# Optimization experiments

Hardware: AMD Instinct MI355X
Metric: run time of the kernel (lower is better)

The kernel has to match this reference:

```python
import jax, jax.numpy as jnp
import numpy as np


def _build_schedule(N, M):
    """Round-robin (circle-method) tournament schedule of Givens rotations.

    Returns per-round, per-row arrays (R=N-1 rounds, each with N/2 disjoint pairs):
      partner[r, n]: row paired with n in round r (self if inactive)
      tpos[r, n]   : flat theta index for the pair (i<j: i*(N-1)-i*(i-1)/2 + j-i-1)
      sign[r, n]   : -1 for the lower-index row i, +1 for j, 0 if inactive
      active[r, n] : 1.0 if row participates in a rotation this round
    Pairs with min(i,j) >= M carry no theta and are skipped (identity).
    """
    assert N % 2 == 0, "even N assumed for the tournament schedule"
    R = N - 1
    players = list(range(N))
    partner = np.tile(np.arange(N, dtype=np.int32), (R, 1))
    tpos = np.zeros((R, N), np.int32)
    sign = np.zeros((R, N), np.float32)
    active = np.zeros((R, N), np.float32)
    for r in range(R):
        for k in range(N // 2):
            a, b = players[k], players[N - 1 - k]
            i, j = (a, b) if a < b else (b, a)
            if i >= M:
                continue
            t = i * (N - 1) - i * (i - 1) // 2 + (j - i - 1)
            partner[r, i], partner[r, j] = j, i
            tpos[r, i] = tpos[r, j] = t
            sign[r, i], sign[r, j] = -1.0, 1.0
            active[r, i] = active[r, j] = 1.0
        players = [players[0], players[-1]] + players[1:-1]
    return (jnp.asarray(partner), jnp.asarray(tpos),
            jnp.asarray(sign), jnp.asarray(active))


def _rotmat_forward(x, thetas, M=None):
    # x: [N, B]; applies the product of Givens rotations G(i,j,theta) round by round.
    N = x.shape[0]
    M = N if M is None else M
    sched = _build_schedule(N, M)

    def body(xc, rd):
        p, t, sg, ac = rd
        th = thetas[t]                       # [N]
        c = jnp.where(ac > 0, jnp.cos(th), 1.0)
        s = sg * jnp.sin(th)                 # 0 where inactive
        # row i: c*x[i] - s*x[j]; row j: s*x[i] + c*x[j]
        return c[:, None] * xc + s[:, None] * xc[p], None

    out, _ = jax.lax.scan(body, x, sched)
    return out


def setup_inputs() -> dict:
    key = jax.random.key(0)
    k1, k2 = jax.random.split(key)
    N, B = 512, 1024
    n_theta = N * (N - 1) // 2  # 130816 (M == N)
    x = jax.random.normal(k1, (N, B), dtype=jnp.float32)
    thetas = jax.random.normal(k2, (n_theta,), dtype=jnp.float32)
    return {"x": x, "thetas": thetas}


def reference(x, thetas):
    return _rotmat_forward(x, thetas)
```

## Files before the change

kernel.cpp:

```cpp
#include <hip/hip_runtime.h>
#include <hip/hip_fp16.h>


#define N_COLS   1024
#define PAIRS    256

typedef __attribute__((ext_vector_type(4))) float f32x4;

__global__ __launch_bounds__(256) void rotmat_setup(const float* __restrict__ thetas,
                                                    __half2* __restrict__ cs16) {
    const int r = blockIdx.x;
    const int k = threadIdx.x;
    int pu = (k == 0) ? 0 : ((k - 1 - r + 1022) % 511) + 1;
    int pv = ((510 - k - r + 1022) % 511) + 1;
    int i = min(pu, pv), j = max(pu, pv);
    int t = i * 511 - (i * (i - 1)) / 2 + (j - i - 1);
    float s, c;
    sincosf(thetas[t], &s, &c);
    float sp = (pu < pv) ? s : -s;
    cs16[r * 256 + k] = __floats2half2_rn(c, sp);
}

__device__ __forceinline__ float dpp_shr1(float old, float src) {
    return __int_as_float(__builtin_amdgcn_update_dpp(
        __float_as_int(old), __float_as_int(src), 0x138, 0xF, 0xF, false));
}
__device__ __forceinline__ float dpp_shl1(float old, float src) {
    return __int_as_float(__builtin_amdgcn_update_dpp(
        __float_as_int(old), __float_as_int(src), 0x130, 0xF, 0xF, false));
}

__device__ __forceinline__ void glds16(const void* g, void* l) {
    __builtin_amdgcn_global_load_lds(
        (const __attribute__((address_space(1))) void*)g,
        (__attribute__((address_space(3))) void*)l, 16, 0, 0);
}

#define FMIX_SN(d, P, x)                                                      \
    asm("v_fma_mix_f32 %0, -%1, %2, 0 op_sel:[1,0,0] op_sel_hi:[1,0,0]"       \
        : "=v"(d) : "v"(P), "v"(x));
#define FMIX_SP(d, P, x)                                                      \
    asm("v_fma_mix_f32 %0, %1, %2, 0 op_sel:[1,0,0] op_sel_hi:[1,0,0]"        \
        : "=v"(d) : "v"(P), "v"(x));
#define FMIX_C(d, P, x, a)                                                    \
    asm("v_fma_mix_f32 %0, %1, %2, %3 op_sel:[0,0,0] op_sel_hi:[1,0,0]"       \
        : "=v"(d) : "v"(P), "v"(x), "v"(a));

#define ROUND(AA)                                                  \
    {                                                              \
        float P0 = (AA).x, P1 = (AA).y, P2 = (AA).z, P3 = (AA).w;  \
        float t3, u3, l3, h3, t0, u0, l0, h0;                      \
        FMIX_SN(t3, P3, hi[3])                                     \
        FMIX_C(l3, P3, lo[3], t3)                                  \
        FMIX_SP(u3, P3, lo[3])                                     \
        FMIX_C(h3, P3, hi[3], u3)                                  \
        FMIX_SN(t0, P0, hi[0])                                     \
        FMIX_C(l0, P0, lo[0], t0)                                  \
        FMIX_SP(u0, P0, lo[0])                                     \
        FMIX_C(h0, P0, hi[0], u0)                                  \
        float nlo0 = dpp_shr1(l0, l3);                             \
        float nhi3 = dpp_shl1(l3, h0);                             \
        float t1, u1, l1, h1, t2, u2, l2, h2;                      \
        FMIX_SN(t1, P1, hi[1])                                     \
        FMIX_C(l1, P1, lo[1], t1)                                  \
        FMIX_SP(u1, P1, lo[1])                                     \
        FMIX_C(h1, P1, hi[1], u1)                                  \
        FMIX_SN(t2, P2, hi[2])                                     \
        FMIX_C(l2, P2, lo[2], t2)                                  \
        FMIX_SP(u2, P2, lo[2])                                     \
        FMIX_C(h2, P2, hi[2], u2)                                  \
        float nlo1 = is0 ? h0 : l0;                                \
        lo[0] = nlo0; lo[1] = nlo1; lo[2] = l1; lo[3] = l2;        \
        hi[0] = h1; hi[1] = h2; hi[2] = h3; hi[3] = nhi3;          \
    }

#define DSRD(dst, addr, imm)                                   \
    asm volatile("ds_read_b128 %0, %1 offset:%c2"              \
                 : "=v"(dst) : "v"(addr), "i"(imm))

#define WL3(a) asm volatile("s_waitcnt lgkmcnt(3)" : "+v"(a))
#define WL2(a) asm volatile("s_waitcnt lgkmcnt(2)" : "+v"(a))
#define WL1(a) asm volatile("s_waitcnt lgkmcnt(1)" : "+v"(a))
#define WL0(a) asm volatile("s_waitcnt lgkmcnt(0)" : "+v"(a))

#define WAITV(n) asm volatile("s_waitcnt vmcnt(" #n ")" ::: "memory")
#define BAR()                               \
    __builtin_amdgcn_s_barrier();           \
    __builtin_amdgcn_sched_barrier(0)

#define STAGE(cix, bix)                                              \
    {                                                                \
        const char* g_ = gsrc + (size_t)(cix)*16384;                 \
        char* l_ = lb + (size_t)(bix)*16384;                         \
        _Pragma("unroll")                                            \
        for (int j = 0; j < 4; ++j)                                  \
            glds16(g_ + j * 1024, l_ + j * 1024);                    \
    }

#define CHUNK16(ACUR, ANXT)                                    \
    WL3(A0); ROUND(A0) DSRD(A0, ACUR,  4 * 1024);              \
    WL3(A1); ROUND(A1) DSRD(A1, ACUR,  5 * 1024);              \
    WL3(A2); ROUND(A2) DSRD(A2, ACUR,  6 * 1024);              \
    WL3(A3); ROUND(A3) DSRD(A3, ACUR,  7 * 1024);              \
    WL3(A0); ROUND(A0) DSRD(A0, ACUR,  8 * 1024);              \
    WL3(A1); ROUND(A1) DSRD(A1, ACUR,  9 * 1024);              \
    WL3(A2); ROUND(A2) DSRD(A2, ACUR, 10 * 1024);              \
    WL3(A3); ROUND(A3) DSRD(A3, ACUR, 11 * 1024);              \
    WL3(A0); ROUND(A0) DSRD(A0, ACUR, 12 * 1024);              \
    WL3(A1); ROUND(A1) DSRD(A1, ACUR, 13 * 1024);              \
    WL3(A2); ROUND(A2) DSRD(A2, ACUR, 14 * 1024);              \
    WL3(A3); ROUND(A3) DSRD(A3, ACUR, 15 * 1024);              \
    WL3(A0); ROUND(A0) DSRD(A0, ANXT,  0 * 1024);              \
    WL3(A1); ROUND(A1) DSRD(A1, ANXT,  1 * 1024);              \
    WL3(A2); ROUND(A2) DSRD(A2, ANXT,  2 * 1024);              \
    WL3(A3); ROUND(A3) DSRD(A3, ANXT,  3 * 1024);

template <bool TAB>
__global__ __launch_bounds__(256, 1) void rotmat_main(const float* __restrict__ x,
                                                      const float* __restrict__ thetas,
                                                      const __half2* __restrict__ cs16,
                                                      float* __restrict__ out) {
    __shared__ f32x4 tab[3 * 1024];

    const int lane = threadIdx.x & 63;
    const int wave = threadIdx.x >> 6;
    const int col  = (blockIdx.x << 2) + wave;
    const int k0   = lane << 2;
    const bool is0 = (lane == 0);

    float lo[4], hi[4];
#pragma unroll
    for (int m = 0; m < 4; ++m) {
        lo[m] = x[(k0 + m) * N_COLS + col];
        hi[m] = x[(511 - k0 - m) * N_COLS + col];
    }

    if constexpr (TAB) {
        const char* gsrc = (const char*)cs16 + (size_t)wave * 4096 + (size_t)lane * 16;
        char* lb = (char*)(&tab[0]) + (size_t)wave * 4096;
        unsigned ldsLane;
        {
            auto p3 = (__attribute__((address_space(3))) char*)(&tab[0]);
            ldsLane = (unsigned)(size_t)p3 + (unsigned)(lane * 16);
        }

        f32x4 A0, A1, A2, A3;

        STAGE(0, 0)
        STAGE(1, 1)
        WAITV(0);
        BAR();
        {
            unsigned a0 = ldsLane;
            DSRD(A0, a0, 0 * 1024);
            DSRD(A1, a0, 1 * 1024);
            DSRD(A2, a0, 2 * 1024);
            DSRD(A3, a0, 3 * 1024);
        }

        int bufCur = 0, bufNxt = 1, bufStg = 2;
        for (int c = 0; c < 30; ++c) {
            WAITV(0);
            BAR();
            STAGE(c + 2, bufStg)
            unsigned aCur = ldsLane + (unsigned)bufCur * 16384u;
            unsigned aNxt = ldsLane + (unsigned)bufNxt * 16384u;
            CHUNK16(aCur, aNxt)
            int t_ = bufCur; bufCur = bufNxt; bufNxt = bufStg; bufStg = t_;
        }

        {
            WAITV(0);
            BAR();
            unsigned aCur = ldsLane + (unsigned)bufCur * 16384u;
            unsigned aNxt = ldsLane + (unsigned)bufNxt * 16384u;
            CHUNK16(aCur, aNxt)
            int t_ = bufCur; bufCur = bufNxt; bufNxt = bufStg; bufStg = t_;
        }

        {
            unsigned aCur = ldsLane + (unsigned)bufCur * 16384u;
            WL3(A0); ROUND(A0) DSRD(A0, aCur,  4 * 1024);
            WL3(A1); ROUND(A1) DSRD(A1, aCur,  5 * 1024);
            WL3(A2); ROUND(A2) DSRD(A2, aCur,  6 * 1024);
            WL3(A3); ROUND(A3) DSRD(A3, aCur,  7 * 1024);
            WL3(A0); ROUND(A0) DSRD(A0, aCur,  8 * 1024);
            WL3(A1); ROUND(A1) DSRD(A1, aCur,  9 * 1024);
            WL3(A2); ROUND(A2) DSRD(A2, aCur, 10 * 1024);
            WL3(A3); ROUND(A3) DSRD(A3, aCur, 11 * 1024);
            WL3(A0); ROUND(A0) DSRD(A0, aCur, 12 * 1024);
            WL3(A1); ROUND(A1) DSRD(A1, aCur, 13 * 1024);
            WL3(A2); ROUND(A2) DSRD(A2, aCur, 14 * 1024);
            WL3(A3); ROUND(A3)
            WL2(A0); ROUND(A0)
            WL1(A1); ROUND(A1)
            WL0(A2); ROUND(A2)
        }
    } else {
        int pu[4], pv[4];
#pragma unroll
        for (int m = 0; m < 4; ++m) {
            pu[m] = (k0 + m == 0) ? 0 : (k0 + m);
            pv[m] = 511 - (k0 + m);
        }
        for (int r = 0; r < 511; ++r) {
            float cc[4], ss[4];
#pragma unroll
            for (int m = 0; m < 4; ++m) {
                int i = min(pu[m], pv[m]), j = max(pu[m], pv[m]);
                int t = i * 511 - (i * (i - 1)) / 2 + (j - i - 1);
                float s, c;
                sincosf(thetas[t], &s, &c);
                cc[m] = c;
                ss[m] = (pu[m] < pv[m]) ? s : -s;
            }
            {
                float t3 = ss[3] * hi[3], u3 = ss[3] * lo[3];
                float l3 = fmaf(cc[3], lo[3], -t3);
                float h3 = fmaf(cc[3], hi[3], u3);
                float t0 = ss[0] * hi[0], u0 = ss[0] * lo[0];
                float l0 = fmaf(cc[0], lo[0], -t0);
                float h0 = fmaf(cc[0], hi[0], u0);
                float nlo0 = dpp_shr1(l0, l3);
                float nhi3 = dpp_shl1(l3, h0);
                float t1 = ss[1] * hi[1], u1 = ss[1] * lo[1];
                float l1 = fmaf(cc[1], lo[1], -t1);
                float h1 = fmaf(cc[1], hi[1], u1);
                float t2 = ss[2] * hi[2], u2 = ss[2] * lo[2];
                float l2 = fmaf(cc[2], lo[2], -t2);
                float h2 = fmaf(cc[2], hi[2], u2);
                float nlo1 = is0 ? h0 : l0;
                lo[0] = nlo0; lo[1] = nlo1; lo[2] = l1; lo[3] = l2;
                hi[0] = h1; hi[1] = h2; hi[2] = h3; hi[3] = nhi3;
            }
#pragma unroll
            for (int m = 0; m < 4; ++m) {
                pu[m] = (k0 + m == 0) ? 0 : ((pu[m] == 1) ? 511 : pu[m] - 1);
                pv[m] = (pv[m] == 1) ? 511 : pv[m] - 1;
            }
        }
    }

#pragma unroll
    for (int m = 0; m < 4; ++m) {
        out[(k0 + m) * N_COLS + col]       = lo[m];
        out[(511 - k0 - m) * N_COLS + col] = hi[m];
    }
}

extern "C" void kernel_launch(void* const* d_in, const int* in_sizes, int n_in,
                              void* d_out, int out_size, void* d_ws, size_t ws_size,
                              hipStream_t stream) {
    const float* x  = (const float*)d_in[0];
    const float* th = (const float*)d_in[1];
    float* out      = (float*)d_out;

    const size_t need = (size_t)512 * 1024;
    if (ws_size >= need) {
        __half2* cs16 = (__half2*)d_ws;
        rotmat_setup<<<511, PAIRS, 0, stream>>>(th, cs16);
        rotmat_main<true><<<N_COLS / 4, 256, 0, stream>>>(x, th, cs16, out);
    } else {
        rotmat_main<false><<<N_COLS / 4, 256, 0, stream>>>(x, th, nullptr, out);
    }
}
```

Baseline: 46.42 us.

## Decompose rotation sequence into two dense orthogonal matrices applied by GEMM

Instead of streaming all 511 rounds of Givens rotations over each of the 1024 columns, the new path builds two 512x512 orthogonal matrices, one per half of the rounds, by running the rotation rounds on identity columns in parallel (1024 waves). It then applies them to x with two fp32 tiled GEMMs, and a final kernel applies the last round directly. The goal is to expose more parallelism than the column-serial main kernel and turn the work into GEMM-shaped compute. The cost is extra kernel launches, an extra intermediate buffer, fp32 GEMM work of about 0.5 GFLOP per pass without matrix cores, and a different rounding order.

```diff
diff --git a/kernel.cpp b/kernel.cpp
--- a/kernel.cpp
+++ b/kernel.cpp
@@ -29,7 +29,6 @@
     return __int_as_float(__builtin_amdgcn_update_dpp(
         __float_as_int(old), __float_as_int(src), 0x130, 0xF, 0xF, false));
 }
-
 __device__ __forceinline__ void glds16(const void* g, void* l) {
     __builtin_amdgcn_global_load_lds(
         (const __attribute__((address_space(1))) void*)g,
@@ -77,12 +76,10 @@
 #define DSRD(dst, addr, imm)                                   \
     asm volatile("ds_read_b128 %0, %1 offset:%c2"              \
                  : "=v"(dst) : "v"(addr), "i"(imm))
-
 #define WL3(a) asm volatile("s_waitcnt lgkmcnt(3)" : "+v"(a))
 #define WL2(a) asm volatile("s_waitcnt lgkmcnt(2)" : "+v"(a))
 #define WL1(a) asm volatile("s_waitcnt lgkmcnt(1)" : "+v"(a))
 #define WL0(a) asm volatile("s_waitcnt lgkmcnt(0)" : "+v"(a))
-
 #define WAITV(n) asm volatile("s_waitcnt vmcnt(" #n ")" ::: "memory")
 #define BAR()                               \
     __builtin_amdgcn_s_barrier();           \
@@ -93,8 +90,8 @@
         const char* g_ = gsrc + (size_t)(cix)*16384;                 \
         char* l_ = lb + (size_t)(bix)*16384;                         \
         _Pragma("unroll")                                            \
-        for (int j = 0; j < 4; ++j)                                  \
-            glds16(g_ + j * 1024, l_ + j * 1024);                    \
+        for (int j_ = 0; j_ < 4; ++j_)                               \
+            glds16(g_ + j_ * 1024, l_ + j_ * 1024);                  \
     }
 
 #define CHUNK16(ACUR, ANXT)                                    \
@@ -115,6 +112,171 @@
     WL3(A2); ROUND(A2) DSRD(A2, ANXT,  2 * 1024);              \
     WL3(A3); ROUND(A3) DSRD(A3, ANXT,  3 * 1024);
 
+#define CHUNK15_TAIL(ACUR)                                     \
+    WL3(A0); ROUND(A0) DSRD(A0, ACUR,  4 * 1024);              \
+    WL3(A1); ROUND(A1) DSRD(A1, ACUR,  5 * 1024);              \
+    WL3(A2); ROUND(A2) DSRD(A2, ACUR,  6 * 1024);              \
+    WL3(A3); ROUND(A3) DSRD(A3, ACUR,  7 * 1024);              \
+    WL3(A0); ROUND(A0) DSRD(A0, ACUR,  8 * 1024);              \
+    WL3(A1); ROUND(A1) DSRD(A1, ACUR,  9 * 1024);              \
+    WL3(A2); ROUND(A2) DSRD(A2, ACUR, 10 * 1024);              \
+    WL3(A3); ROUND(A3) DSRD(A3, ACUR, 11 * 1024);              \
+    WL3(A0); ROUND(A0) DSRD(A0, ACUR, 12 * 1024);              \
+    WL3(A1); ROUND(A1) DSRD(A1, ACUR, 13 * 1024);              \
+    WL3(A2); ROUND(A2) DSRD(A2, ACUR, 14 * 1024);              \
+    WL3(A3); ROUND(A3)                                         \
+    WL2(A0); ROUND(A0)                                         \
+    WL1(A1); ROUND(A1)                                         \
+    WL0(A2); ROUND(A2)
+
+__device__ __forceinline__ int player_of(int r, int p) {
+    return (p == 0) ? 0 : ((p - 1 - r + 1022) % 511) + 1;
+}
+
+__global__ __launch_bounds__(256, 1) void rotmat_build(const __half2* __restrict__ cs16,
+                                                       float* __restrict__ qt) {
+    __shared__ f32x4 tab[3 * 1024];
+
+    const int lane = threadIdx.x & 63;
+    const int wave = threadIdx.x >> 6;
+    const int wid  = (blockIdx.x << 2) + wave;
+    const int seg  = wid >> 9;
+    const int j    = wid & 511;
+    const int r0   = seg ? 255 : 0;
+    const int k0   = lane << 2;
+    const bool is0 = (lane == 0);
+
+    float lo[4], hi[4];
+#pragma unroll
+    for (int m = 0; m < 4; ++m) {
+        int p = k0 + m, pq = 511 - p;
+        lo[m] = (player_of(r0, p) == j) ? 1.0f : 0.0f;
+        hi[m] = (player_of(r0, pq) == j) ? 1.0f : 0.0f;
+    }
+
+    const char* gsrc = (const char*)cs16 + (size_t)r0 * 1024
+                     + (size_t)wave * 4096 + (size_t)lane * 16;
+    char* lb = (char*)(&tab[0]) + (size_t)wave * 4096;
+    unsigned ldsLane;
+    {
+        auto p3 = (__attribute__((address_space(3))) char*)(&tab[0]);
+        ldsLane = (unsigned)(size_t)p3 + (unsigned)(lane * 16);
+    }
+
+    f32x4 A0, A1, A2, A3;
+
+    STAGE(0, 0)
+    STAGE(1, 1)
+    WAITV(0);
+    BAR();
+    {
+        unsigned a0 = ldsLane;
+        DSRD(A0, a0, 0 * 1024);
+        DSRD(A1, a0, 1 * 1024);
+        DSRD(A2, a0, 2 * 1024);
+        DSRD(A3, a0, 3 * 1024);
+    }
+
+    int bufCur = 0, bufNxt = 1, bufStg = 2;
+    for (int c = 0; c < 14; ++c) {
+        WAITV(0);
+        BAR();
+        STAGE(c + 2, bufStg)
+        unsigned aCur = ldsLane + (unsigned)bufCur * 16384u;
+        unsigned aNxt = ldsLane + (unsigned)bufNxt * 16384u;
+        CHUNK16(aCur, aNxt)
+        int t_ = bufCur; bufCur = bufNxt; bufNxt = bufStg; bufStg = t_;
+    }
+    {
+        WAITV(0);
+        BAR();
+        unsigned aCur = ldsLane + (unsigned)bufCur * 16384u;
+        unsigned aNxt = ldsLane + (unsigned)bufNxt * 16384u;
+        CHUNK16(aCur, aNxt)
+        int t_ = bufCur; bufCur = bufNxt; bufNxt = bufStg; bufStg = t_;
+    }
+    {
+        unsigned aCur = ldsLane + (unsigned)bufCur * 16384u;
+        CHUNK15_TAIL(aCur)
+    }
+
+    const int r1 = seg ? 510 : 255;
+    float* qv = qt + (size_t)seg * 262144 + (size_t)j * 512;
+#pragma unroll
+    for (int m = 0; m < 4; ++m) {
+        int p = k0 + m, pq = 511 - p;
+        qv[player_of(r1, p)]  = lo[m];
+        qv[player_of(r1, pq)] = hi[m];
+    }
+}
+
+__global__ __launch_bounds__(256) void gemm_qt(const float* __restrict__ AT,
+                                               const float* __restrict__ B,
+                                               float* __restrict__ C) {
+    __shared__ float As[32][32];
+    __shared__ float Bs[32][64];
+
+    const int t    = threadIdx.x;
+    const int bx   = blockIdx.x & 15;
+    const int by   = blockIdx.x >> 4;
+    const int row0 = by * 32, col0 = bx * 64;
+    const int mr   = (t & 15) * 2;
+    const int nc   = (t >> 4) * 4;
+
+    float acc00 = 0, acc01 = 0, acc02 = 0, acc03 = 0;
+    float acc10 = 0, acc11 = 0, acc12 = 0, acc13 = 0;
+
+    for (int kt = 0; kt < 16; ++kt) {
+        __syncthreads();
+        {
+            int kk = t >> 3, mm = (t & 7) * 4;
+            *(float4*)&As[kk][mm] =
+                *(const float4*)&AT[(size_t)(kt * 32 + kk) * 512 + row0 + mm];
+        }
+        {
+            int kk = t >> 4, cc = (t & 15) * 4;
+            *(float4*)&Bs[kk][cc] =
+                *(const float4*)&B[(size_t)(kt * 32 + kk) * 1024 + col0 + cc];
+            *(float4*)&Bs[kk + 16][cc] =
+                *(const float4*)&B[(size_t)(kt * 32 + kk + 16) * 1024 + col0 + cc];
+        }
+        __syncthreads();
+#pragma unroll
+        for (int kk = 0; kk < 32; ++kk) {
+            float a0 = As[kk][mr], a1 = As[kk][mr + 1];
+            float4 b = *(float4*)&Bs[kk][nc];
+            acc00 = fmaf(a0, b.x, acc00); acc01 = fmaf(a0, b.y, acc01);
+            acc02 = fmaf(a0, b.z, acc02); acc03 = fmaf(a0, b.w, acc03);
+            acc10 = fmaf(a1, b.x, acc10); acc11 = fmaf(a1, b.y, acc11);
+            acc12 = fmaf(a1, b.z, acc12); acc13 = fmaf(a1, b.w, acc13);
+        }
+    }
+    *(float4*)&C[(size_t)(row0 + mr) * 1024 + col0 + nc] =
+        make_float4(acc00, acc01, acc02, acc03);
+    *(float4*)&C[(size_t)(row0 + mr + 1) * 1024 + col0 + nc] =
+        make_float4(acc10, acc11, acc12, acc13);
+}
+
+__global__ __launch_bounds__(256) void round_last(const float* __restrict__ thetas,
+                                                  float* __restrict__ out) {
+    const int k = blockIdx.x;
+    int pu = (k == 0) ? 0 : ((k - 1 - 510 + 1022) % 511) + 1;
+    int pv = ((510 - k - 510 + 1022) % 511) + 1;
+    int i = min(pu, pv), jj = max(pu, pv);
+    int t = i * 511 - (i * (i - 1)) / 2 + (jj - i - 1);
+    float s, c;
+    sincosf(thetas[t], &s, &c);
+    float* ri = out + (size_t)i * 1024;
+    float* rj = out + (size_t)jj * 1024;
+#pragma unroll
+    for (int u = 0; u < 4; ++u) {
+        int col = threadIdx.x + u * 256;
+        float a = ri[col], b = rj[col];
+        ri[col] = fmaf(c, a, -(s * b));
+        rj[col] = fmaf(s, a, c * b);
+    }
+}
+
 template <bool TAB>
 __global__ __launch_bounds__(256, 1) void rotmat_main(const float* __restrict__ x,
                                                       const float* __restrict__ thetas,
@@ -143,9 +305,7 @@
             auto p3 = (__attribute__((address_space(3))) char*)(&tab[0]);
             ldsLane = (unsigned)(size_t)p3 + (unsigned)(lane * 16);
         }
-
         f32x4 A0, A1, A2, A3;
-
         STAGE(0, 0)
         STAGE(1, 1)
         WAITV(0);
@@ -157,7 +317,6 @@
             DSRD(A2, a0, 2 * 1024);
             DSRD(A3, a0, 3 * 1024);
         }
-
         int bufCur = 0, bufNxt = 1, bufStg = 2;
         for (int c = 0; c < 30; ++c) {
             WAITV(0);
@@ -168,7 +327,6 @@
             CHUNK16(aCur, aNxt)
             int t_ = bufCur; bufCur = bufNxt; bufNxt = bufStg; bufStg = t_;
         }
-
         {
             WAITV(0);
             BAR();
@@ -177,24 +335,9 @@
             CHUNK16(aCur, aNxt)
             int t_ = bufCur; bufCur = bufNxt; bufNxt = bufStg; bufStg = t_;
         }
-
         {
             unsigned aCur = ldsLane + (unsigned)bufCur * 16384u;
-            WL3(A0); ROUND(A0) DSRD(A0, aCur,  4 * 1024);
-            WL3(A1); ROUND(A1) DSRD(A1, aCur,  5 * 1024);
-            WL3(A2); ROUND(A2) DSRD(A2, aCur,  6 * 1024);
-            WL3(A3); ROUND(A3) DSRD(A3, aCur,  7 * 1024);
-            WL3(A0); ROUND(A0) DSRD(A0, aCur,  8 * 1024);
-            WL3(A1); ROUND(A1) DSRD(A1, aCur,  9 * 1024);
-            WL3(A2); ROUND(A2) DSRD(A2, aCur, 10 * 1024);
-            WL3(A3); ROUND(A3) DSRD(A3, aCur, 11 * 1024);
-            WL3(A0); ROUND(A0) DSRD(A0, aCur, 12 * 1024);
-            WL3(A1); ROUND(A1) DSRD(A1, aCur, 13 * 1024);
-            WL3(A2); ROUND(A2) DSRD(A2, aCur, 14 * 1024);
-            WL3(A3); ROUND(A3)
-            WL2(A0); ROUND(A0)
-            WL1(A1); ROUND(A1)
-            WL0(A2); ROUND(A2)
+            CHUNK15_TAIL(aCur)
         }
     } else {
         int pu[4], pv[4];
@@ -207,8 +350,8 @@
             float cc[4], ss[4];
 #pragma unroll
             for (int m = 0; m < 4; ++m) {
-                int i = min(pu[m], pv[m]), j = max(pu[m], pv[m]);
-                int t = i * 511 - (i * (i - 1)) / 2 + (j - i - 1);
+                int i = min(pu[m], pv[m]), jj = max(pu[m], pv[m]);
+                int t = i * 511 - (i * (i - 1)) / 2 + (jj - i - 1);
                 float s, c;
                 sincosf(thetas[t], &s, &c);
                 cc[m] = c;
@@ -255,8 +398,21 @@
     const float* th = (const float*)d_in[1];
     float* out      = (float*)d_out;
 
-    const size_t need = (size_t)512 * 1024;
-    if (ws_size >= need) {
+    const size_t TAB_B = (size_t)512 * 1024;
+    const size_t Q_B   = (size_t)512 * 512 * 4;
+    const size_t Y_B   = (size_t)512 * 1024 * 4;
+    const size_t need_decomp = TAB_B + 2 * Q_B + Y_B;
+
+    if (ws_size >= need_decomp) {
+        __half2* cs16 = (__half2*)d_ws;
+        float* qt = (float*)((char*)d_ws + TAB_B);
+        float* Y  = (float*)((char*)d_ws + TAB_B + 2 * Q_B);
+        rotmat_setup<<<511, PAIRS, 0, stream>>>(th, cs16);
+        rotmat_build<<<256, 256, 0, stream>>>(cs16, qt);
+        gemm_qt<<<256, 256, 0, stream>>>(qt, x, Y);
+        gemm_qt<<<256, 256, 0, stream>>>(qt + 262144, Y, out);
+        round_last<<<256, 256, 0, stream>>>(th, out);
+    } else if (ws_size >= TAB_B) {
         __half2* cs16 = (__half2*)d_ws;
         rotmat_setup<<<511, PAIRS, 0, stream>>>(th, cs16);
         rotmat_main<true><<<N_COLS / 4, 256, 0, stream>>>(x, th, cs16, out);
```

Result: slower. 69.34 us (+49.4%).
